# Optimization experiments

Hardware: AMD Instinct MI355X
Metric: run time of the kernel (lower is better)

Reference implementation:

```python
import jax, jax.numpy as jnp
import numpy as np

EMBED_DIM = 1024
NUM_HEADS = 16
D_K = EMBED_DIM // NUM_HEADS


def setup_inputs() -> dict:
    key = jax.random.key(0)
    ks = jax.random.split(key, 5)
    s = 1.0 / np.sqrt(EMBED_DIM)  # roughly match nn.Linear init scale
    return {
        "x": jax.random.normal(ks[0], (2, 2048, EMBED_DIM), dtype=jnp.float32),
        "wq": jax.random.normal(ks[1], (EMBED_DIM, EMBED_DIM), dtype=jnp.float32) * s,
        "wk": jax.random.normal(ks[2], (EMBED_DIM, EMBED_DIM), dtype=jnp.float32) * s,
        "wv": jax.random.normal(ks[3], (EMBED_DIM, EMBED_DIM), dtype=jnp.float32) * s,
        "wo": jax.random.normal(ks[4], (EMBED_DIM, EMBED_DIM), dtype=jnp.float32) * s,
    }


def reference(x, wq, wk, wv, wo):
    b, s, e = x.shape
    # nn.Linear(bias=False): y = x @ W.T
    def split_heads(t):
        return t.reshape(b, s, NUM_HEADS, D_K).transpose(0, 2, 1, 3)  # [b,h,s,d]
    q = split_heads(x @ wq.T)
    k = split_heads(x @ wk.T)
    v = split_heads(x @ wv.T)
    scores = jnp.einsum("bhqd,bhkd->bhqk", q, k) / jnp.sqrt(jnp.float32(D_K))
    attn = jax.nn.softmax(scores, axis=-1)
    out = jnp.einsum("bhqk,bhkd->bhqd", attn, v)  # [b,h,s,d]
    out = out.transpose(0, 2, 1, 3).reshape(b, s, e)
    return out @ wo.T
```

## Files before the change

kernel.cpp:

```cpp
#include <hip/hip_runtime.h>
#include <stdint.h>

typedef unsigned short u16;
typedef float f32x4 __attribute__((ext_vector_type(4)));
typedef __bf16 bf16x8 __attribute__((ext_vector_type(8)));
typedef short s16x4 __attribute__((ext_vector_type(4)));

__device__ __forceinline__ u16 f2bf(float f) {
  union { float f; uint32_t u; } c; c.f = f;
  uint32_t u = c.u;
  u += 0x7fffu + ((u >> 16) & 1u);
  return (u16)(u >> 16);
}

__device__ __forceinline__ uint32_t pkbf(float a, float b) {
  union { float f; uint32_t u; } ua, ub; ua.f = a; ub.f = b;
  return __builtin_amdgcn_perm(ub.u, ua.u, 0x07060302u);
}

#define GLOAD_LDS16(g, l)                                                              \
  __builtin_amdgcn_global_load_lds((__attribute__((address_space(1))) void*)(g),       \
                                   (__attribute__((address_space(3))) void*)(l), 16, 0, 0)

__global__ __launch_bounds__(256) void cvt_all(const float* __restrict__ x,
                                               const float* __restrict__ wq,
                                               const float* __restrict__ wk,
                                               const float* __restrict__ wv,
                                               const float* __restrict__ wo,
                                               u16* __restrict__ xb,
                                               u16* __restrict__ wqkvb,
                                               u16* __restrict__ wob) {
  int bx = blockIdx.x;
  const float* src;
  u16* dst;
  int i;
  if (bx < 4096) {
    src = x; dst = xb; i = bx * 256 + threadIdx.x;
  } else {
    int r = bx - 4096;
    int w = r >> 10;
    i = (r & 1023) * 256 + threadIdx.x;
    if (w == 0)      { src = wq; dst = wqkvb; }
    else if (w == 1) { src = wk; dst = wqkvb + 1048576; }
    else if (w == 2) { src = wv; dst = wqkvb + 2097152; }
    else             { src = wo; dst = wob; }
  }
  const float4 v = ((const float4*)src)[i];
  ushort4 o;
  o.x = f2bf(v.x); o.y = f2bf(v.y); o.z = f2bf(v.z); o.w = f2bf(v.w);
  ((ushort4*)dst)[i] = o;
}

__global__ __launch_bounds__(256, 3) void gemm_qkv(const u16* __restrict__ A,
                                                   const u16* __restrict__ B,
                                                   u16* __restrict__ QKb,
                                                   u16* __restrict__ Vt) {
  const int K = 1024;
  __shared__ __align__(16) u16 sA[3 * 4096];
  __shared__ __align__(16) u16 sB[3 * 4096];
  const int tid = threadIdx.x;
  const int lane = tid & 63;
  const int wave = tid >> 6;
  const int quad = lane >> 4, l16 = lane & 15;
  const int wm = (wave >> 1) * 64, wn = (wave & 1) * 64;
  const int bm = blockIdx.y * 128, bn = blockIdx.x * 128;

  f32x4 acc[4][4];
#pragma unroll
  for (int i = 0; i < 4; i++)
#pragma unroll
    for (int j = 0; j < 4; j++) acc[i][j] = (f32x4){0.f, 0.f, 0.f, 0.f};

#define QKV_STAGE(t, bi)                                                           \
  {                                                                                \
    const int k0s = (t) * 32;                                                      \
    char* dA = (char*)(sA + (bi) * 4096);                                          \
    char* dB = (char*)(sB + (bi) * 4096);                                          \
    _Pragma("unroll")                                                              \
    for (int k2 = 0; k2 < 2; k2++) {                                               \
      int u = k2 * 256 + tid;                                                      \
      int row = u >> 2, c4 = (u & 3) ^ (row & 3);                                  \
      GLOAD_LDS16(A + (size_t)(bm + row) * K + k0s + c4 * 8, dA + u * 16);         \
      GLOAD_LDS16(B + (size_t)(bn + row) * K + k0s + c4 * 8, dB + u * 16);         \
    }                                                                              \
  }

  QKV_STAGE(0, 0);
  QKV_STAGE(1, 1);

  int cur = 0, stg = 2;
  for (int T = 0; T < 32; ++T) {
    if (T < 31) asm volatile("s_waitcnt vmcnt(4)" ::: "memory");
    else        asm volatile("s_waitcnt vmcnt(0)" ::: "memory");
    __builtin_amdgcn_s_barrier();
    asm volatile("" ::: "memory");
    if (T < 30) QKV_STAGE(T + 2, stg);

    const u16* cA = sA + cur * 4096;
    const u16* cB = sB + cur * 4096;
    bf16x8 af[4], bfr[4];
#pragma unroll
    for (int mt = 0; mt < 4; mt++) {
      int ra = wm + mt * 16 + l16;
      af[mt] = *(const bf16x8*)&cA[ra * 32 + ((quad ^ (ra & 3)) * 8)];
    }
#pragma unroll
    for (int nt = 0; nt < 4; nt++) {
      int rb = wn + nt * 16 + l16;
      bfr[nt] = *(const bf16x8*)&cB[rb * 32 + ((quad ^ (rb & 3)) * 8)];
    }
#pragma unroll
    for (int mt = 0; mt < 4; mt++)
#pragma unroll
      for (int nt = 0; nt < 4; nt++)
        acc[mt][nt] = __builtin_amdgcn_mfma_f32_16x16x32_bf16(af[mt], bfr[nt], acc[mt][nt], 0, 0, 0);

    cur = (cur == 2) ? 0 : cur + 1;
    stg = (stg == 2) ? 0 : stg + 1;
  }
#undef QKV_STAGE

  if (blockIdx.x < 16) {
    const float qs = (blockIdx.x < 8) ? 0.18033688011f : 1.0f;
#pragma unroll
    for (int mt = 0; mt < 4; mt++)
#pragma unroll
      for (int nt = 0; nt < 4; nt++)
#pragma unroll
        for (int r = 0; r < 4; r++) {
          int row = bm + wm + mt * 16 + quad * 4 + r;
          int col = bn + wn + nt * 16 + l16;
          QKb[(size_t)row * 2048 + col] = f2bf(acc[mt][nt][r] * qs);
        }
  } else {
#pragma unroll
    for (int mt = 0; mt < 4; mt++)
#pragma unroll
      for (int nt = 0; nt < 4; nt++) {
        int hd = (bn - 2048) + wn + nt * 16 + l16;
        int tok = bm + wm + mt * 16 + quad * 4;
        ushort4 o;
        o.x = f2bf(acc[mt][nt][0]);
        o.y = f2bf(acc[mt][nt][1]);
        o.z = f2bf(acc[mt][nt][2]);
        o.w = f2bf(acc[mt][nt][3]);
        *(ushort4*)&Vt[(size_t)hd * 4096 + tok] = o;
      }
  }
}

__global__ __launch_bounds__(256, 2) void attn_fwd(const u16* __restrict__ QKb,
                                                   const u16* __restrict__ Vt,
                                                   u16* __restrict__ O) {
  const int bx = blockIdx.x;
  const int qt = bx >> 5;
  const int h  = (bx >> 1) & 15;
  const int b  = bx & 1;
  const int tid = threadIdx.x;
  const int lane = tid & 63;
  const int wave = tid >> 6;
  const int quad = lane >> 4, l16 = lane & 15;

  __shared__ __align__(16) u16 smem[32768];
  u16* sQ = smem;
  u16* sK = smem + 8192;
  u16* sV = smem + 20480;

  const int tok0 = b * 2048;
  const int q0 = qt * 128;
  const int colh = h * 64;

#pragma unroll
  for (int k2 = 0; k2 < 4; k2++) {
    int c = k2 * 256 + tid;
    int row = c >> 3, c8 = (c & 7) ^ (row & 7);
    GLOAD_LDS16(QKb + (size_t)(tok0 + q0 + row) * 2048 + colh + c8 * 8,
                (char*)sQ + c * 16);
  }
#pragma unroll
  for (int t = 0; t < 2; t++) {
#pragma unroll
    for (int k2 = 0; k2 < 2; k2++) {
      int c = k2 * 256 + tid;
      int row = c >> 3, c8 = (c & 7) ^ (row & 7);
      GLOAD_LDS16(QKb + (size_t)(tok0 + t * 64 + row) * 2048 + 1024 + colh + c8 * 8,
                  (char*)(sK + t * 4096) + c * 16);
      GLOAD_LDS16(Vt + (size_t)(colh + row) * 4096 + tok0 + t * 64 + c8 * 8,
                  (char*)(sV + t * 4096) + c * 16);
    }
  }
  asm volatile("s_waitcnt vmcnt(8)" ::: "memory");
  __builtin_amdgcn_s_barrier();
  asm volatile("" ::: "memory");

  bf16x8 aq[2][2];
#pragma unroll
  for (int sub = 0; sub < 2; sub++)
#pragma unroll
    for (int kh = 0; kh < 2; kh++) {
      int rq = wave * 32 + sub * 16 + l16;
      aq[sub][kh] = *(const bf16x8*)&sQ[rq * 64 + (((kh * 4 + quad) ^ (rq & 7)) * 8)];
    }

  f32x4 oacc[2][4];
  float lsum[2] = {0.f, 0.f};
#pragma unroll
  for (int sub = 0; sub < 2; sub++)
#pragma unroll
    for (int db = 0; db < 4; db++) oacc[sub][db] = (f32x4){0.f, 0.f, 0.f, 0.f};

  int cur = 0, stg = 2;
  for (int it = 0; it < 32; ++it) {
    if (it < 31) asm volatile("s_waitcnt vmcnt(4)" ::: "memory");
    else         asm volatile("s_waitcnt vmcnt(0)" ::: "memory");
    __builtin_amdgcn_s_barrier();
    asm volatile("" ::: "memory");
    if (it < 30) {
      const int nkv = (it + 2) * 64;
      char* sKn = (char*)(sK + stg * 4096);
      char* sVn = (char*)(sV + stg * 4096);
#pragma unroll
      for (int k2 = 0; k2 < 2; k2++) {
        int c = k2 * 256 + tid;
        int row = c >> 3, c8 = (c & 7) ^ (row & 7);
        GLOAD_LDS16(QKb + (size_t)(tok0 + nkv + row) * 2048 + 1024 + colh + c8 * 8,
                    sKn + c * 16);
        GLOAD_LDS16(Vt + (size_t)(colh + row) * 4096 + tok0 + nkv + c8 * 8,
                    sVn + c * 16);
      }
    }
    const u16* sKc = sK + cur * 4096;
    const u16* sVc = sV + cur * 4096;

    bf16x8 kf[4][2];
#pragma unroll
    for (int nt = 0; nt < 4; nt++)
#pragma unroll
      for (int kh = 0; kh < 2; kh++) {
        int rr = nt * 16 + l16;
        kf[nt][kh] = *(const bf16x8*)&sKc[rr * 64 + (((kh * 4 + quad) ^ (rr & 7)) * 8)];
      }
    s16x4 vf[4][4];
#pragma unroll
    for (int db = 0; db < 4; db++)
#pragma unroll
      for (int nt = 0; nt < 4; nt++) {
        int row = db * 16 + l16;
        int c16 = (nt * 2 + (quad >> 1)) ^ (row & 7);
        vf[db][nt] = *(const s16x4*)&sVc[row * 64 + c16 * 8 + (quad & 1) * 4];
      }

#pragma unroll
    for (int sub = 0; sub < 2; sub++) {
      float e[4][4];
#pragma unroll
      for (int nt = 0; nt < 4; nt++) {
        f32x4 c = (f32x4){0.f, 0.f, 0.f, 0.f};
        c = __builtin_amdgcn_mfma_f32_16x16x32_bf16(kf[nt][0], aq[sub][0], c, 0, 0, 0);
        c = __builtin_amdgcn_mfma_f32_16x16x32_bf16(kf[nt][1], aq[sub][1], c, 0, 0, 0);
#pragma unroll
        for (int r = 0; r < 4; r++) e[nt][r] = __builtin_amdgcn_exp2f(c[r]);
        lsum[sub] += (e[nt][0] + e[nt][1]) + (e[nt][2] + e[nt][3]);
      }
#pragma unroll
      for (int nt = 0; nt < 4; nt++) {
        union { uint32_t u[2]; s16x4 v; } bb;
        bb.u[0] = pkbf(e[nt][0], e[nt][1]);
        bb.u[1] = pkbf(e[nt][2], e[nt][3]);
#pragma unroll
        for (int db = 0; db < 4; db++)
          oacc[sub][db] = __builtin_amdgcn_mfma_f32_16x16x16bf16_1k(vf[db][nt], bb.v, oacc[sub][db], 0, 0, 0);
      }
    }
    cur = (cur == 2) ? 0 : cur + 1;
    stg = (stg == 2) ? 0 : stg + 1;
  }

#pragma unroll
  for (int sub = 0; sub < 2; sub++) {
    float v = lsum[sub];
    v += __shfl_xor(v, 16, 64);
    v += __shfl_xor(v, 32, 64);
    lsum[sub] = 1.0f / v;
  }

  u16* sT = smem + wave * 2176;
#pragma unroll
  for (int sub = 0; sub < 2; sub++)
#pragma unroll
    for (int db = 0; db < 4; db++)
#pragma unroll
      for (int r = 0; r < 4; r++)
        sT[(sub * 16 + l16) * 68 + db * 16 + quad * 4 + r] = f2bf(oacc[sub][db][r] * lsum[sub]);
#pragma unroll
  for (int k = 0; k < 4; k++) {
    int qrow = k * 8 + (lane >> 3);
    int cch = lane & 7;
    uint4 vrow = *(const uint4*)&sT[qrow * 68 + cch * 8];
    int tokr = tok0 + q0 + wave * 32 + qrow;
    *(uint4*)&O[(size_t)tokr * 1024 + colh + cch * 8] = vrow;
  }
}

__global__ __launch_bounds__(256) void gemm_out(const u16* __restrict__ A,
                                                const u16* __restrict__ B,
                                                float* __restrict__ C) {
  const int N = 1024, K = 1024;
  __shared__ __align__(16) u16 sA[3 * 4096];
  __shared__ __align__(16) u16 sB[3 * 2048];
  const int tid = threadIdx.x;
  const int lane = tid & 63;
  const int wave = tid >> 6;
  const int quad = lane >> 4, l16 = lane & 15;
  const int wm = (wave >> 1) * 64, wn = (wave & 1) * 32;
  const int bm = blockIdx.y * 128, bn = blockIdx.x * 64;

  f32x4 acc[4][2];
#pragma unroll
  for (int i = 0; i < 4; i++)
#pragma unroll
    for (int j = 0; j < 2; j++) acc[i][j] = (f32x4){0.f, 0.f, 0.f, 0.f};

#define OUT_STAGE(t, bi)                                                           \
  {                                                                                \
    const int k0s = (t) * 32;                                                      \
    char* dA = (char*)(sA + (bi) * 4096);                                          \
    char* dB = (char*)(sB + (bi) * 2048);                                          \
    _Pragma("unroll")                                                              \
    for (int k2 = 0; k2 < 2; k2++) {                                               \
      int u = k2 * 256 + tid;                                                      \
      int row = u >> 2, c4 = (u & 3) ^ (row & 3);                                  \
      GLOAD_LDS16(A + (size_t)(bm + row) * K + k0s + c4 * 8, dA + u * 16);         \
    }                                                                              \
    {                                                                              \
      int u = tid;                                                                 \
      int row = u >> 2, c4 = (u & 3) ^ (row & 3);                                  \
      GLOAD_LDS16(B + (size_t)(bn + row) * K + k0s + c4 * 8, dB + u * 16);         \
    }                                                                              \
  }

  OUT_STAGE(0, 0);
  OUT_STAGE(1, 1);

  int cur = 0, stg = 2;
  for (int T = 0; T < 32; ++T) {
    if (T < 31) asm volatile("s_waitcnt vmcnt(3)" ::: "memory");
    else        asm volatile("s_waitcnt vmcnt(0)" ::: "memory");
    __builtin_amdgcn_s_barrier();
    asm volatile("" ::: "memory");
    if (T < 30) OUT_STAGE(T + 2, stg);

    const u16* cA = sA + cur * 4096;
    const u16* cB = sB + cur * 2048;
    bf16x8 af[4], bfr[2];
#pragma unroll
    for (int mt = 0; mt < 4; mt++) {
      int ra = wm + mt * 16 + l16;
      af[mt] = *(const bf16x8*)&cA[ra * 32 + ((quad ^ (ra & 3)) * 8)];
    }
#pragma unroll
    for (int nt = 0; nt < 2; nt++) {
      int rb = wn + nt * 16 + l16;
      bfr[nt] = *(const bf16x8*)&cB[rb * 32 + ((quad ^ (rb & 3)) * 8)];
    }
#pragma unroll
    for (int mt = 0; mt < 4; mt++)
#pragma unroll
      for (int nt = 0; nt < 2; nt++)
        acc[mt][nt] = __builtin_amdgcn_mfma_f32_16x16x32_bf16(af[mt], bfr[nt], acc[mt][nt], 0, 0, 0);

    cur = (cur == 2) ? 0 : cur + 1;
    stg = (stg == 2) ? 0 : stg + 1;
  }
#undef OUT_STAGE

#pragma unroll
  for (int mt = 0; mt < 4; mt++)
#pragma unroll
    for (int nt = 0; nt < 2; nt++)
#pragma unroll
      for (int r = 0; r < 4; r++) {
        int row = bm + wm + mt * 16 + quad * 4 + r;
        int col = bn + wn + nt * 16 + l16;
        C[(size_t)row * N + col] = acc[mt][nt][r];
      }
}

extern "C" void kernel_launch(void* const* d_in, const int* in_sizes, int n_in,
                              void* d_out, int out_size, void* d_ws, size_t ws_size,
                              hipStream_t stream) {
  const float* x  = (const float*)d_in[0];
  const float* wq = (const float*)d_in[1];
  const float* wk = (const float*)d_in[2];
  const float* wv = (const float*)d_in[3];
  const float* wo = (const float*)d_in[4];
  float* out = (float*)d_out;
  char* ws = (char*)d_ws;
  const size_t MB = 1u << 20;

  u16* xb    = (u16*)(ws);
  u16* wqkvb = (u16*)(ws + 8 * MB);
  u16* wob   = (u16*)(ws + 14 * MB);
  u16* QKb   = (u16*)(ws + 16 * MB);
  u16* Vtb   = (u16*)(ws + 32 * MB);
  u16* Ob    = xb;

  cvt_all<<<8192, 256, 0, stream>>>(x, wq, wk, wv, wo, xb, wqkvb, wob);

  gemm_qkv<<<dim3(24, 32), 256, 0, stream>>>(xb, wqkvb, QKb, Vtb);

  attn_fwd<<<512, 256, 0, stream>>>(QKb, Vtb, Ob);

  gemm_out<<<dim3(16, 32), 256, 0, stream>>>(Ob, wob, out);
}
```

Measured before the change: 178.6 us.

## Split attention KV tile across waves and reduce partial outputs through LDS

Each wave now processes all 128 query rows of the block but only a 16-key slice of every 64-key K/V tile, instead of owning 32 query rows across the whole tile. Each wave therefore reads a quarter of the K/V fragments from LDS per iteration, which targets LDS read bandwidth in the inner loop. In exchange every wave holds 8x more Q fragments and output accumulators in registers, which raises register pressure and spill risk. The partial outputs and row sums must also be combined across the four waves through LDS with several extra barriers in the epilogue.

New measurement: 183.2 us. +2.6%, slower.

```diff
diff --git a/kernel.cpp b/kernel.cpp
--- a/kernel.cpp
+++ b/kernel.cpp
@@ -165,6 +165,9 @@
   u16* sQ = smem;
   u16* sK = smem + 8192;
   u16* sV = smem + 20480;
+  float* R0 = (float*)smem;
+  float* R1 = (float*)(smem + 16384);
+  float* lsumT = (float*)smem;
 
   const int tok0 = b * 2048;
   const int q0 = qt * 128;
@@ -193,21 +196,23 @@
   __builtin_amdgcn_s_barrier();
   asm volatile("" ::: "memory");
 
-  bf16x8 aq[2][2];
-#pragma unroll
-  for (int sub = 0; sub < 2; sub++)
+  bf16x8 aq[8][2];
+#pragma unroll
+  for (int sub = 0; sub < 8; sub++)
 #pragma unroll
     for (int kh = 0; kh < 2; kh++) {
-      int rq = wave * 32 + sub * 16 + l16;
+      int rq = sub * 16 + l16;
       aq[sub][kh] = *(const bf16x8*)&sQ[rq * 64 + (((kh * 4 + quad) ^ (rq & 7)) * 8)];
     }
 
-  f32x4 oacc[2][4];
-  float lsum[2] = {0.f, 0.f};
-#pragma unroll
-  for (int sub = 0; sub < 2; sub++)
+  f32x4 oacc[8][4];
+  float lsum[8];
+#pragma unroll
+  for (int sub = 0; sub < 8; sub++) {
+    lsum[sub] = 0.f;
 #pragma unroll
     for (int db = 0; db < 4; db++) oacc[sub][db] = (f32x4){0.f, 0.f, 0.f, 0.f};
+  }
 
   int cur = 0, stg = 2;
   for (int it = 0; it < 32; ++it) {
@@ -232,73 +237,108 @@
     const u16* sKc = sK + cur * 4096;
     const u16* sVc = sV + cur * 4096;
 
-    bf16x8 kf[4][2];
-#pragma unroll
-    for (int nt = 0; nt < 4; nt++)
-#pragma unroll
-      for (int kh = 0; kh < 2; kh++) {
-        int rr = nt * 16 + l16;
-        kf[nt][kh] = *(const bf16x8*)&sKc[rr * 64 + (((kh * 4 + quad) ^ (rr & 7)) * 8)];
-      }
-    s16x4 vf[4][4];
-#pragma unroll
-    for (int db = 0; db < 4; db++)
-#pragma unroll
-      for (int nt = 0; nt < 4; nt++) {
-        int row = db * 16 + l16;
-        int c16 = (nt * 2 + (quad >> 1)) ^ (row & 7);
-        vf[db][nt] = *(const s16x4*)&sVc[row * 64 + c16 * 8 + (quad & 1) * 4];
-      }
-
-#pragma unroll
-    for (int sub = 0; sub < 2; sub++) {
-      float e[4][4];
-#pragma unroll
-      for (int nt = 0; nt < 4; nt++) {
-        f32x4 c = (f32x4){0.f, 0.f, 0.f, 0.f};
-        c = __builtin_amdgcn_mfma_f32_16x16x32_bf16(kf[nt][0], aq[sub][0], c, 0, 0, 0);
-        c = __builtin_amdgcn_mfma_f32_16x16x32_bf16(kf[nt][1], aq[sub][1], c, 0, 0, 0);
-#pragma unroll
-        for (int r = 0; r < 4; r++) e[nt][r] = __builtin_amdgcn_exp2f(c[r]);
-        lsum[sub] += (e[nt][0] + e[nt][1]) + (e[nt][2] + e[nt][3]);
-      }
-#pragma unroll
-      for (int nt = 0; nt < 4; nt++) {
-        union { uint32_t u[2]; s16x4 v; } bb;
-        bb.u[0] = pkbf(e[nt][0], e[nt][1]);
-        bb.u[1] = pkbf(e[nt][2], e[nt][3]);
-#pragma unroll
-        for (int db = 0; db < 4; db++)
-          oacc[sub][db] = __builtin_amdgcn_mfma_f32_16x16x16bf16_1k(vf[db][nt], bb.v, oacc[sub][db], 0, 0, 0);
-      }
+    bf16x8 kf[2];
+#pragma unroll
+    for (int kh = 0; kh < 2; kh++) {
+      int rr = wave * 16 + l16;
+      kf[kh] = *(const bf16x8*)&sKc[rr * 64 + (((kh * 4 + quad) ^ (rr & 7)) * 8)];
+    }
+    s16x4 vf[4];
+#pragma unroll
+    for (int db = 0; db < 4; db++) {
+      int row = db * 16 + l16;
+      int c16 = (wave * 2 + (quad >> 1)) ^ (row & 7);
+      vf[db] = *(const s16x4*)&sVc[row * 64 + c16 * 8 + (quad & 1) * 4];
+    }
+
+#pragma unroll
+    for (int sub = 0; sub < 8; sub++) {
+      f32x4 c = (f32x4){0.f, 0.f, 0.f, 0.f};
+      c = __builtin_amdgcn_mfma_f32_16x16x32_bf16(kf[0], aq[sub][0], c, 0, 0, 0);
+      c = __builtin_amdgcn_mfma_f32_16x16x32_bf16(kf[1], aq[sub][1], c, 0, 0, 0);
+      float e0 = __builtin_amdgcn_exp2f(c[0]);
+      float e1 = __builtin_amdgcn_exp2f(c[1]);
+      float e2 = __builtin_amdgcn_exp2f(c[2]);
+      float e3 = __builtin_amdgcn_exp2f(c[3]);
+      lsum[sub] += (e0 + e1) + (e2 + e3);
+      union { uint32_t u[2]; s16x4 v; } bb;
+      bb.u[0] = pkbf(e0, e1);
+      bb.u[1] = pkbf(e2, e3);
+#pragma unroll
+      for (int db = 0; db < 4; db++)
+        oacc[sub][db] = __builtin_amdgcn_mfma_f32_16x16x16bf16_1k(vf[db], bb.v, oacc[sub][db], 0, 0, 0);
     }
     cur = (cur == 2) ? 0 : cur + 1;
     stg = (stg == 2) ? 0 : stg + 1;
   }
 
-#pragma unroll
-  for (int sub = 0; sub < 2; sub++) {
+  asm volatile("s_waitcnt lgkmcnt(0)" ::: "memory");
+  __builtin_amdgcn_s_barrier();
+
+#pragma unroll
+  for (int sub = 0; sub < 8; sub++) {
     float v = lsum[sub];
     v += __shfl_xor(v, 16, 64);
     v += __shfl_xor(v, 32, 64);
-    lsum[sub] = 1.0f / v;
-  }
-
-  u16* sT = smem + wave * 2176;
-#pragma unroll
-  for (int sub = 0; sub < 2; sub++)
-#pragma unroll
-    for (int db = 0; db < 4; db++)
-#pragma unroll
-      for (int r = 0; r < 4; r++)
-        sT[(sub * 16 + l16) * 68 + db * 16 + quad * 4 + r] = f2bf(oacc[sub][db][r] * lsum[sub]);
-#pragma unroll
-  for (int k = 0; k < 4; k++) {
-    int qrow = k * 8 + (lane >> 3);
-    int cch = lane & 7;
-    uint4 vrow = *(const uint4*)&sT[qrow * 68 + cch * 8];
-    int tokr = tok0 + q0 + wave * 32 + qrow;
-    *(uint4*)&O[(size_t)tokr * 1024 + colh + cch * 8] = vrow;
+    lsum[sub] = v;
+  }
+  if (quad == 0) {
+#pragma unroll
+    for (int sub = 0; sub < 8; sub++)
+      lsumT[wave * 128 + sub * 16 + l16] = lsum[sub];
+  }
+  __builtin_amdgcn_s_barrier();
+  float rtot[2];
+#pragma unroll
+  for (int j = 0; j < 2; j++) {
+    int so = wave * 2 + j;
+    float t = lsumT[0 * 128 + so * 16 + l16] + lsumT[1 * 128 + so * 16 + l16] +
+              lsumT[2 * 128 + so * 16 + l16] + lsumT[3 * 128 + so * 16 + l16];
+    rtot[j] = 1.0f / t;
+  }
+  __builtin_amdgcn_s_barrier();
+
+  if (wave < 2) {
+    float* R = wave ? R1 : R0;
+#pragma unroll
+    for (int sub = 0; sub < 8; sub++)
+#pragma unroll
+      for (int db = 0; db < 4; db++) {
+        int q = sub * 16 + l16;
+        int d = db * 16 + quad * 4;
+        *(f32x4*)&R[q * 64 + (d ^ ((q & 7) << 3))] = oacc[sub][db];
+      }
+  }
+  __builtin_amdgcn_s_barrier();
+  if (wave >= 2) {
+    float* R = (wave == 3) ? R1 : R0;
+#pragma unroll
+    for (int sub = 0; sub < 8; sub++)
+#pragma unroll
+      for (int db = 0; db < 4; db++) {
+        int q = sub * 16 + l16;
+        int d = db * 16 + quad * 4;
+        float* p = &R[q * 64 + (d ^ ((q & 7) << 3))];
+        *(f32x4*)p = *(const f32x4*)p + oacc[sub][db];
+      }
+  }
+  __builtin_amdgcn_s_barrier();
+#pragma unroll
+  for (int j = 0; j < 2; j++) {
+    int sub = wave * 2 + j;
+    int q = sub * 16 + l16;
+#pragma unroll
+    for (int db = 0; db < 4; db++) {
+      int d = db * 16 + quad * 4;
+      int loc = q * 64 + (d ^ ((q & 7) << 3));
+      f32x4 o = *(const f32x4*)&R0[loc] + *(const f32x4*)&R1[loc];
+      ushort4 st;
+      st.x = f2bf(o[0] * rtot[j]);
+      st.y = f2bf(o[1] * rtot[j]);
+      st.z = f2bf(o[2] * rtot[j]);
+      st.w = f2bf(o[3] * rtot[j]);
+      *(ushort4*)&O[(size_t)(tok0 + q0 + q) * 1024 + colh + d] = st;
+    }
   }
 }
 
```

## Split attention KV tile across wave pairs with LDS reduction of partial outputs

Applied to the files above, without the earlier changes.

Reorganizes the attention kernel so each wave handles 64 query rows but only half of each 64-key tile. Two waves then combine their partial output accumulators and row sums through shared memory at the end. This halves the per-wave K/V fragment loads from LDS and reuses each K/V fragment across four query sub-tiles, at the cost of more accumulator registers and a final cross-wave reduction with extra barriers. The epilogue now writes bf16 output directly to global memory in 8-byte pieces instead of staging it through LDS for coalesced 16-byte stores.

New measurement: 179.4 us. Within noise of the previous version (+0.5%).

```diff
diff --git a/kernel.cpp b/kernel.cpp
--- a/kernel.cpp
+++ b/kernel.cpp
@@ -159,6 +159,8 @@
   const int tid = threadIdx.x;
   const int lane = tid & 63;
   const int wave = tid >> 6;
+  const int wq = wave >> 1;
+  const int wk = wave & 1;
   const int quad = lane >> 4, l16 = lane & 15;
 
   __shared__ __align__(16) u16 smem[32768];
@@ -193,21 +195,23 @@
   __builtin_amdgcn_s_barrier();
   asm volatile("" ::: "memory");
 
-  bf16x8 aq[2][2];
-#pragma unroll
-  for (int sub = 0; sub < 2; sub++)
+  bf16x8 aq[4][2];
+#pragma unroll
+  for (int sub = 0; sub < 4; sub++)
 #pragma unroll
     for (int kh = 0; kh < 2; kh++) {
-      int rq = wave * 32 + sub * 16 + l16;
+      int rq = wq * 64 + sub * 16 + l16;
       aq[sub][kh] = *(const bf16x8*)&sQ[rq * 64 + (((kh * 4 + quad) ^ (rq & 7)) * 8)];
     }
 
-  f32x4 oacc[2][4];
-  float lsum[2] = {0.f, 0.f};
-#pragma unroll
-  for (int sub = 0; sub < 2; sub++)
+  f32x4 oacc[4][4];
+  float lsum[4];
+#pragma unroll
+  for (int sub = 0; sub < 4; sub++) {
+    lsum[sub] = 0.f;
 #pragma unroll
     for (int db = 0; db < 4; db++) oacc[sub][db] = (f32x4){0.f, 0.f, 0.f, 0.f};
+  }
 
   int cur = 0, stg = 2;
   for (int it = 0; it < 32; ++it) {
@@ -232,41 +236,39 @@
     const u16* sKc = sK + cur * 4096;
     const u16* sVc = sV + cur * 4096;
 
-    bf16x8 kf[4][2];
-#pragma unroll
-    for (int nt = 0; nt < 4; nt++)
+    bf16x8 kf[2][2];
+#pragma unroll
+    for (int nt = 0; nt < 2; nt++)
 #pragma unroll
       for (int kh = 0; kh < 2; kh++) {
-        int rr = nt * 16 + l16;
+        int rr = wk * 32 + nt * 16 + l16;
         kf[nt][kh] = *(const bf16x8*)&sKc[rr * 64 + (((kh * 4 + quad) ^ (rr & 7)) * 8)];
       }
-    s16x4 vf[4][4];
+    s16x4 vf[4][2];
 #pragma unroll
     for (int db = 0; db < 4; db++)
 #pragma unroll
-      for (int nt = 0; nt < 4; nt++) {
+      for (int nt = 0; nt < 2; nt++) {
         int row = db * 16 + l16;
-        int c16 = (nt * 2 + (quad >> 1)) ^ (row & 7);
+        int c16 = ((wk * 2 + nt) * 2 + (quad >> 1)) ^ (row & 7);
         vf[db][nt] = *(const s16x4*)&sVc[row * 64 + c16 * 8 + (quad & 1) * 4];
       }
 
 #pragma unroll
-    for (int sub = 0; sub < 2; sub++) {
-      float e[4][4];
-#pragma unroll
-      for (int nt = 0; nt < 4; nt++) {
+    for (int sub = 0; sub < 4; sub++) {
+#pragma unroll
+      for (int nt = 0; nt < 2; nt++) {
         f32x4 c = (f32x4){0.f, 0.f, 0.f, 0.f};
         c = __builtin_amdgcn_mfma_f32_16x16x32_bf16(kf[nt][0], aq[sub][0], c, 0, 0, 0);
         c = __builtin_amdgcn_mfma_f32_16x16x32_bf16(kf[nt][1], aq[sub][1], c, 0, 0, 0);
-#pragma unroll
-        for (int r = 0; r < 4; r++) e[nt][r] = __builtin_amdgcn_exp2f(c[r]);
-        lsum[sub] += (e[nt][0] + e[nt][1]) + (e[nt][2] + e[nt][3]);
-      }
-#pragma unroll
-      for (int nt = 0; nt < 4; nt++) {
+        float e0 = __builtin_amdgcn_exp2f(c[0]);
+        float e1 = __builtin_amdgcn_exp2f(c[1]);
+        float e2 = __builtin_amdgcn_exp2f(c[2]);
+        float e3 = __builtin_amdgcn_exp2f(c[3]);
+        lsum[sub] += (e0 + e1) + (e2 + e3);
         union { uint32_t u[2]; s16x4 v; } bb;
-        bb.u[0] = pkbf(e[nt][0], e[nt][1]);
-        bb.u[1] = pkbf(e[nt][2], e[nt][3]);
+        bb.u[0] = pkbf(e0, e1);
+        bb.u[1] = pkbf(e2, e3);
 #pragma unroll
         for (int db = 0; db < 4; db++)
           oacc[sub][db] = __builtin_amdgcn_mfma_f32_16x16x16bf16_1k(vf[db][nt], bb.v, oacc[sub][db], 0, 0, 0);
@@ -276,29 +278,50 @@
     stg = (stg == 2) ? 0 : stg + 1;
   }
 
-#pragma unroll
-  for (int sub = 0; sub < 2; sub++) {
+  asm volatile("s_waitcnt lgkmcnt(0)" ::: "memory");
+  __builtin_amdgcn_s_barrier();
+
+#pragma unroll
+  for (int sub = 0; sub < 4; sub++) {
     float v = lsum[sub];
     v += __shfl_xor(v, 16, 64);
     v += __shfl_xor(v, 32, 64);
-    lsum[sub] = 1.0f / v;
-  }
-
-  u16* sT = smem + wave * 2176;
-#pragma unroll
-  for (int sub = 0; sub < 2; sub++)
-#pragma unroll
-    for (int db = 0; db < 4; db++)
-#pragma unroll
-      for (int r = 0; r < 4; r++)
-        sT[(sub * 16 + l16) * 68 + db * 16 + quad * 4 + r] = f2bf(oacc[sub][db][r] * lsum[sub]);
-#pragma unroll
-  for (int k = 0; k < 4; k++) {
-    int qrow = k * 8 + (lane >> 3);
-    int cch = lane & 7;
-    uint4 vrow = *(const uint4*)&sT[qrow * 68 + cch * 8];
-    int tokr = tok0 + q0 + wave * 32 + qrow;
-    *(uint4*)&O[(size_t)tokr * 1024 + colh + cch * 8] = vrow;
+    lsum[sub] = v;
+  }
+
+  float* Rbase = (float*)((char*)smem + wq * 16384);
+  float* lsumT = (float*)((char*)smem + 32768);
+
+  if (wk == 0) {
+#pragma unroll
+    for (int sub = 0; sub < 4; sub++) {
+#pragma unroll
+      for (int db = 0; db < 4; db++) {
+        int q = sub * 16 + l16;
+        int d = db * 16 + quad * 4;
+        *(f32x4*)&Rbase[q * 64 + (d ^ ((q & 7) << 3))] = oacc[sub][db];
+      }
+      if (quad == 0) lsumT[wq * 64 + sub * 16 + l16] = lsum[sub];
+    }
+  }
+  __builtin_amdgcn_s_barrier();
+  if (wk == 1) {
+#pragma unroll
+    for (int sub = 0; sub < 4; sub++) {
+      int q = sub * 16 + l16;
+      float rt = 1.0f / (lsum[sub] + lsumT[wq * 64 + q]);
+#pragma unroll
+      for (int db = 0; db < 4; db++) {
+        int d = db * 16 + quad * 4;
+        f32x4 o = *(const f32x4*)&Rbase[q * 64 + (d ^ ((q & 7) << 3))] + oacc[sub][db];
+        ushort4 st;
+        st.x = f2bf(o[0] * rt);
+        st.y = f2bf(o[1] * rt);
+        st.z = f2bf(o[2] * rt);
+        st.w = f2bf(o[3] * rt);
+        *(ushort4*)&O[(size_t)(tok0 + q0 + wq * 64 + q) * 1024 + colh + d] = st;
+      }
+    }
   }
 }
 
```

## Halve attention query tile, double-buffer K/V, and remap blocks for occupancy

Applied to the files above, without the earlier changes.

The attention kernel now handles 64 query rows per block instead of 128, giving one 16-row subtile per wave and launching 1024 blocks instead of 512. It replaces the triple-buffered K/V prefetch with double buffering, which shrinks shared memory and raises the launch bound to 4 blocks per CU. Block indices are remapped so that neighbouring blocks share a head/batch pair, aiming at better L2 reuse of K/V. The cost is that each K/V tile is loaded and turned into fragments twice as often per query row, and the pipeline now waits for the next tile to fully land (vmcnt 0) at the end of every iteration.

Result: slower. 184.7 us (+3.4%).

```diff
diff --git a/kernel.cpp b/kernel.cpp
--- a/kernel.cpp
+++ b/kernel.cpp
@@ -149,76 +149,66 @@
   }
 }
 
-__global__ __launch_bounds__(256, 2) void attn_fwd(const u16* __restrict__ QKb,
+__global__ __launch_bounds__(256, 4) void attn_fwd(const u16* __restrict__ QKb,
                                                    const u16* __restrict__ Vt,
                                                    u16* __restrict__ O) {
   const int bx = blockIdx.x;
-  const int qt = bx >> 5;
-  const int h  = (bx >> 1) & 15;
-  const int b  = bx & 1;
+  const int pair = (bx & 7) * 4 + (bx >> 8);
+  const int qt   = (bx >> 3) & 31;
+  const int h = pair >> 1;
+  const int b = pair & 1;
   const int tid = threadIdx.x;
   const int lane = tid & 63;
   const int wave = tid >> 6;
   const int quad = lane >> 4, l16 = lane & 15;
 
-  __shared__ __align__(16) u16 smem[32768];
+  __shared__ __align__(16) u16 smem[20480];
   u16* sQ = smem;
-  u16* sK = smem + 8192;
-  u16* sV = smem + 20480;
+  u16* sK = smem + 4096;
+  u16* sV = smem + 12288;
 
   const int tok0 = b * 2048;
-  const int q0 = qt * 128;
+  const int q0 = qt * 64;
   const int colh = h * 64;
 
 #pragma unroll
-  for (int k2 = 0; k2 < 4; k2++) {
+  for (int k2 = 0; k2 < 2; k2++) {
     int c = k2 * 256 + tid;
     int row = c >> 3, c8 = (c & 7) ^ (row & 7);
     GLOAD_LDS16(QKb + (size_t)(tok0 + q0 + row) * 2048 + colh + c8 * 8,
                 (char*)sQ + c * 16);
   }
 #pragma unroll
-  for (int t = 0; t < 2; t++) {
-#pragma unroll
-    for (int k2 = 0; k2 < 2; k2++) {
-      int c = k2 * 256 + tid;
-      int row = c >> 3, c8 = (c & 7) ^ (row & 7);
-      GLOAD_LDS16(QKb + (size_t)(tok0 + t * 64 + row) * 2048 + 1024 + colh + c8 * 8,
-                  (char*)(sK + t * 4096) + c * 16);
-      GLOAD_LDS16(Vt + (size_t)(colh + row) * 4096 + tok0 + t * 64 + c8 * 8,
-                  (char*)(sV + t * 4096) + c * 16);
-    }
-  }
-  asm volatile("s_waitcnt vmcnt(8)" ::: "memory");
+  for (int k2 = 0; k2 < 2; k2++) {
+    int c = k2 * 256 + tid;
+    int row = c >> 3, c8 = (c & 7) ^ (row & 7);
+    GLOAD_LDS16(QKb + (size_t)(tok0 + row) * 2048 + 1024 + colh + c8 * 8,
+                (char*)sK + c * 16);
+    GLOAD_LDS16(Vt + (size_t)(colh + row) * 4096 + tok0 + c8 * 8,
+                (char*)sV + c * 16);
+  }
+  asm volatile("s_waitcnt vmcnt(0)" ::: "memory");
   __builtin_amdgcn_s_barrier();
   asm volatile("" ::: "memory");
 
-  bf16x8 aq[2][2];
-#pragma unroll
-  for (int sub = 0; sub < 2; sub++)
-#pragma unroll
-    for (int kh = 0; kh < 2; kh++) {
-      int rq = wave * 32 + sub * 16 + l16;
-      aq[sub][kh] = *(const bf16x8*)&sQ[rq * 64 + (((kh * 4 + quad) ^ (rq & 7)) * 8)];
-    }
-
-  f32x4 oacc[2][4];
-  float lsum[2] = {0.f, 0.f};
-#pragma unroll
-  for (int sub = 0; sub < 2; sub++)
-#pragma unroll
-    for (int db = 0; db < 4; db++) oacc[sub][db] = (f32x4){0.f, 0.f, 0.f, 0.f};
-
-  int cur = 0, stg = 2;
+  bf16x8 aq[2];
+#pragma unroll
+  for (int kh = 0; kh < 2; kh++) {
+    int rq = wave * 16 + l16;
+    aq[kh] = *(const bf16x8*)&sQ[rq * 64 + (((kh * 4 + quad) ^ (rq & 7)) * 8)];
+  }
+
+  f32x4 oacc[4];
+  float lsum = 0.f;
+#pragma unroll
+  for (int db = 0; db < 4; db++) oacc[db] = (f32x4){0.f, 0.f, 0.f, 0.f};
+
   for (int it = 0; it < 32; ++it) {
-    if (it < 31) asm volatile("s_waitcnt vmcnt(4)" ::: "memory");
-    else         asm volatile("s_waitcnt vmcnt(0)" ::: "memory");
-    __builtin_amdgcn_s_barrier();
-    asm volatile("" ::: "memory");
-    if (it < 30) {
-      const int nkv = (it + 2) * 64;
-      char* sKn = (char*)(sK + stg * 4096);
-      char* sVn = (char*)(sV + stg * 4096);
+    const int cur = it & 1;
+    if (it < 31) {
+      const int nkv = (it + 1) * 64;
+      char* sKn = (char*)(sK + (cur ^ 1) * 4096);
+      char* sVn = (char*)(sV + (cur ^ 1) * 4096);
 #pragma unroll
       for (int k2 = 0; k2 < 2; k2++) {
         int c = k2 * 256 + tid;
@@ -251,53 +241,46 @@
       }
 
 #pragma unroll
-    for (int sub = 0; sub < 2; sub++) {
-      float e[4][4];
-#pragma unroll
-      for (int nt = 0; nt < 4; nt++) {
-        f32x4 c = (f32x4){0.f, 0.f, 0.f, 0.f};
-        c = __builtin_amdgcn_mfma_f32_16x16x32_bf16(kf[nt][0], aq[sub][0], c, 0, 0, 0);
-        c = __builtin_amdgcn_mfma_f32_16x16x32_bf16(kf[nt][1], aq[sub][1], c, 0, 0, 0);
-#pragma unroll
-        for (int r = 0; r < 4; r++) e[nt][r] = __builtin_amdgcn_exp2f(c[r]);
-        lsum[sub] += (e[nt][0] + e[nt][1]) + (e[nt][2] + e[nt][3]);
-      }
-#pragma unroll
-      for (int nt = 0; nt < 4; nt++) {
-        union { uint32_t u[2]; s16x4 v; } bb;
-        bb.u[0] = pkbf(e[nt][0], e[nt][1]);
-        bb.u[1] = pkbf(e[nt][2], e[nt][3]);
-#pragma unroll
-        for (int db = 0; db < 4; db++)
-          oacc[sub][db] = __builtin_amdgcn_mfma_f32_16x16x16bf16_1k(vf[db][nt], bb.v, oacc[sub][db], 0, 0, 0);
-      }
-    }
-    cur = (cur == 2) ? 0 : cur + 1;
-    stg = (stg == 2) ? 0 : stg + 1;
-  }
-
-#pragma unroll
-  for (int sub = 0; sub < 2; sub++) {
-    float v = lsum[sub];
+    for (int nt = 0; nt < 4; nt++) {
+      f32x4 c = (f32x4){0.f, 0.f, 0.f, 0.f};
+      c = __builtin_amdgcn_mfma_f32_16x16x32_bf16(kf[nt][0], aq[0], c, 0, 0, 0);
+      c = __builtin_amdgcn_mfma_f32_16x16x32_bf16(kf[nt][1], aq[1], c, 0, 0, 0);
+      float e0 = __builtin_amdgcn_exp2f(c[0]);
+      float e1 = __builtin_amdgcn_exp2f(c[1]);
+      float e2 = __builtin_amdgcn_exp2f(c[2]);
+      float e3 = __builtin_amdgcn_exp2f(c[3]);
+      lsum += (e0 + e1) + (e2 + e3);
+      union { uint32_t u[2]; s16x4 v; } bb;
+      bb.u[0] = pkbf(e0, e1);
+      bb.u[1] = pkbf(e2, e3);
+#pragma unroll
+      for (int db = 0; db < 4; db++)
+        oacc[db] = __builtin_amdgcn_mfma_f32_16x16x16bf16_1k(vf[db][nt], bb.v, oacc[db], 0, 0, 0);
+    }
+    asm volatile("s_waitcnt vmcnt(0)" ::: "memory");
+    __builtin_amdgcn_s_barrier();
+    asm volatile("" ::: "memory");
+  }
+
+  {
+    float v = lsum;
     v += __shfl_xor(v, 16, 64);
     v += __shfl_xor(v, 32, 64);
-    lsum[sub] = 1.0f / v;
-  }
-
-  u16* sT = smem + wave * 2176;
-#pragma unroll
-  for (int sub = 0; sub < 2; sub++)
-#pragma unroll
-    for (int db = 0; db < 4; db++)
-#pragma unroll
-      for (int r = 0; r < 4; r++)
-        sT[(sub * 16 + l16) * 68 + db * 16 + quad * 4 + r] = f2bf(oacc[sub][db][r] * lsum[sub]);
-#pragma unroll
-  for (int k = 0; k < 4; k++) {
+    lsum = 1.0f / v;
+  }
+
+  u16* sT = smem + wave * 1152;
+#pragma unroll
+  for (int db = 0; db < 4; db++)
+#pragma unroll
+    for (int r = 0; r < 4; r++)
+      sT[l16 * 72 + db * 16 + quad * 4 + r] = f2bf(oacc[db][r] * lsum);
+#pragma unroll
+  for (int k = 0; k < 2; k++) {
     int qrow = k * 8 + (lane >> 3);
     int cch = lane & 7;
-    uint4 vrow = *(const uint4*)&sT[qrow * 68 + cch * 8];
-    int tokr = tok0 + q0 + wave * 32 + qrow;
+    uint4 vrow = *(const uint4*)&sT[qrow * 72 + cch * 8];
+    int tokr = tok0 + q0 + wave * 16 + qrow;
     *(uint4*)&O[(size_t)tokr * 1024 + colh + cch * 8] = vrow;
   }
 }
@@ -409,7 +392,7 @@
 
   gemm_qkv<<<dim3(24, 32), 256, 0, stream>>>(xb, wqkvb, QKb, Vtb);
 
-  attn_fwd<<<512, 256, 0, stream>>>(QKb, Vtb, Ob);
+  attn_fwd<<<1024, 256, 0, stream>>>(QKb, Vtb, Ob);
 
   gemm_out<<<dim3(16, 32), 256, 0, stream>>>(Ob, wob, out);
 }
```
